# Optimization experiments

Hardware: AMD Instinct MI355X
Metric: run time of the kernel (lower is better)

## Reference

```python
import jax, jax.numpy as jnp
import numpy as np

B = 262144      # batch of Monte Carlo paths
D = 5           # number of assets
NSTEPS = 20     # Euler-Maruyama steps
H = 0.1         # T / N
R = 0.06        # risk-free rate
T = 2.0
SIGMA = 0.2     # vol (same for all assets)
B_DRIFT = 0.1   # P-measure drift
CURTAGE = 0.005
SQRT_H = float(np.sqrt(H))


def setup_inputs() -> dict:
    key = jax.random.key(0)
    ks = jax.random.split(key, 10)
    sc = 0.1  # weight init scale
    return {
        "x_in": jax.random.uniform(ks[0], (B, 1), dtype=jnp.float32),
        "dW": jax.random.normal(ks[1], (NSTEPS, B, D), dtype=jnp.float32) * SQRT_H,
        "Wo": jax.random.normal(ks[2], (1, 2 * D + 1), dtype=jnp.float32) * sc,
        "bo": jnp.zeros((2 * D + 1,), jnp.float32),
        "Wk": jax.random.normal(ks[3], (1, 2 * D), dtype=jnp.float32) * sc,
        "bk": jnp.zeros((2 * D,), jnp.float32),
        "Wu0": jax.random.normal(ks[4], (1, D), dtype=jnp.float32) * sc,
        "bu0": jnp.zeros((D,), jnp.float32),
        "W1": jax.random.normal(ks[5], (NSTEPS - 1, 1, 20), dtype=jnp.float32) * sc,
        "b1": jnp.zeros((NSTEPS - 1, 20), jnp.float32),
        "W2": jax.random.normal(ks[6], (NSTEPS - 1, 20, 20), dtype=jnp.float32) * sc,
        "b2": jnp.zeros((NSTEPS - 1, 20), jnp.float32),
        "W3": jax.random.normal(ks[7], (NSTEPS - 1, 20, D), dtype=jnp.float32) * sc,
        "b3": jnp.zeros((NSTEPS - 1, D), jnp.float32),
    }


def _mlp(x, w1, c1, w2, c2, w3, c3):
    # SubNetwork: Dense(20) relu -> Dense(20) relu -> Dense(D) linear
    h1 = jax.nn.relu(x @ w1 + c1)
    h2 = jax.nn.relu(h1 @ w2 + c2)
    return h2 @ w3 + c3


def _forward(x_in, dW, Wo, bo, Wk, bk, Wu0, bu0, W1, b1, W2, b2, W3, b3):
    b_vec = jnp.full((D,), B_DRIFT, dtype=x_in.dtype)
    x = x_in                                             # wealth [B,1]
    alpha_options = jax.nn.softmax(x @ Wo + bo, axis=-1)[:, : 2 * D]
    alpha_options_tot = jnp.mean(jnp.sum(alpha_options, axis=1))
    K = 1.0 + 0.25 * jnp.tanh(x @ Wk + bk)               # strikes [B,2D]
    rescale = 1.0 - alpha_options_tot
    alpha = x @ Wu0 + bu0                                # linear head, [B,D]

    S = jnp.ones((x.shape[0], D), dtype=x.dtype)         # P-measure asset prices
    S_Q = S                                              # Q-measure asset prices
    dN_acu = jnp.zeros((x.shape[0], D), dtype=x.dtype)
    N_m1 = None

    for n in range(1, NSTEPS + 1):   # fixed small unrolled rollout
        u = alpha                                        # dollar allocation per asset
        N_p = u / S                                      # number of shares
        if n > 1:
            dN_acu = dN_acu + jnp.abs(N_p - N_m1)        # turnover accumulator
        N_m1 = N_p
        dWn = dW[n - 1]
        # wealth Euler step: risk-free on cash + risky exposure (GBM, no jumps)
        x = x + (x - jnp.sum(u, axis=1, keepdims=True)) * (R * H) \
              + jnp.sum(u * (b_vec * H + SIGMA * dWn), axis=1, keepdims=True)
        S = S * (1.0 + b_vec * H + SIGMA * dWn)
        S_Q = S_Q * (1.0 + R * H + SIGMA * dWn)
        if n < NSTEPS:
            alpha = _mlp(x, W1[n - 1], b1[n - 1], W2[n - 1], b2[n - 1],
                         W3[n - 1], b3[n - 1])

    dN = jnp.sum(dN_acu, axis=1, keepdims=True)          # [B,1]
    disc = jnp.exp(-R * T)
    C0 = disc * jnp.mean(jnp.maximum(S_Q - K[:, :D], 0.0), axis=0)   # [D] MC call price
    P0 = disc * jnp.mean(jnp.maximum(K[:, D:] - S_Q, 0.0), axis=0)   # [D] MC put price
    C_T = jnp.maximum(S - K[:, :D], 0.0) / (C0 + 1e-8)
    P_T = jnp.maximum(K[:, D:] - S, 0.0) / (P0 + 1e-8)
    del P_T  # options_in_p=False: puts/calls not added to wealth

    x = x - CURTAGE * dN                                 # transaction costs

    p5 = jnp.percentile(x, 5.0)
    p95 = jnp.percentile(x, 95.0)
    m_lo = x < p5
    m_hi = x > p95
    cnt_lo = jnp.maximum(jnp.sum(m_lo), 1).astype(x.dtype)
    cnt_hi = jnp.maximum(jnp.sum(m_hi), 1).astype(x.dtype)

    loss1 = -jnp.mean(x)
    loss2 = jnp.var(x)
    loss3 = -jnp.sum(jnp.where(m_lo, x, 0.0)) / cnt_lo   # -CVaR_5 tail mean
    loss4 = -jnp.sum(jnp.where(m_hi, x, 0.0)) / cnt_hi
    loss5 = jnp.mean(C_T[:, 0])
    loss6 = K[0, 1]
    loss7 = jnp.asarray(rescale, x.dtype)
    return (loss1, loss2, loss3, loss4, loss5, loss6, loss7)


def reference(x_in, dW, Wo, bo, Wk, bk, Wu0, bu0, W1, b1, W2, b2, W3, b3):
    losses = _forward(x_in, dW, Wo, bo, Wk, bk, Wu0, bu0,
                      W1, b1, W2, b2, W3, b3)
    return tuple(jnp.reshape(l, (1,)) for l in losses)
```

## Files before the change

### kernel.cpp

```cpp
#include <hip/hip_runtime.h>
#include <math.h>

#define BB 262144
#define NST 20
#define RHc 0.006f
#define BHc 0.01f
#define SIGc 0.2f
#define CURTc 0.005f
#define DISCf 0.8869204367171575f

#define P 4
#define THB 256
#define NBLK_SIM 256
#define CH 65536

#define H1_BLK 32
#define H1_THR 1024
#define W_BLK 256
#define W_THR 256

#define SIMP_OFF  BB
#define TAILP_OFF (SIMP_OFF + NBLK_SIM * 5)
#define ICTRL     (TAILP_OFF + W_BLK * 4)
#define H2_OFF 0
#define H3_OFF 8192
#define CNT_OFF 12288
#define ST_OFF  12296
#define SF_OFF  12320
#define ZTOT    12289
#define H1R_OFF 12352

__device__ __forceinline__ unsigned fkey(float f) {
    unsigned u = __float_as_uint(f);
    return (u & 0x80000000u) ? ~u : (u | 0x80000000u);
}
__device__ __forceinline__ float funkey(unsigned k) {
    return __uint_as_float((k & 0x80000000u) ? (k ^ 0x80000000u) : ~k);
}
__device__ __forceinline__ float wred(float v) {
#pragma unroll
    for (int o = 32; o > 0; o >>= 1) v += __shfl_down(v, o);
    return v;
}
__device__ __forceinline__ unsigned short f2bf(float f) {
    unsigned u = __float_as_uint(f);
    unsigned r = u + 0x7fffu + ((u >> 16) & 1u);
    return (unsigned short)(r >> 16);
}

__global__ void zero_kernel(int* __restrict__ ctrl) {
    int i = blockIdx.x * blockDim.x + threadIdx.x;
    if (i < ZTOT) ctrl[i] = 0;
}

#define STRD 416
#define HB   (19 * STRD)

__global__ __launch_bounds__(THB, 1) void sim_kernel(
    const float* __restrict__ x_in, const float* __restrict__ dW,
    const float* __restrict__ Wo, const float* __restrict__ bo,
    const float* __restrict__ Wk, const float* __restrict__ bk,
    const float* __restrict__ Wu0, const float* __restrict__ bu0,
    const float* __restrict__ W1, const float* __restrict__ b1,
    const float* __restrict__ W2, const float* __restrict__ b2,
    const float* __restrict__ W3, const float* __restrict__ b3,
    float* __restrict__ ws, int* __restrict__ ctrl, float* __restrict__ out)
{
    __shared__ float L[HB + 40];
    __shared__ float red[4][5];
    __shared__ int lastF;
    const int tid = threadIdx.x;

    for (int t = tid; t < 19 * 20; t += THB) {
        int s = t / 20, j = t % 20;
        L[s * STRD + j]      = W1[t];
        L[s * STRD + 20 + j] = b1[t];
        L[s * STRD + 40 + j] = b2[t];
    }
    for (int t = tid; t < 19 * 100; t += THB) {
        int s = t / 100, r = t % 100, i = r / 5, k = r % 5;
        L[s * STRD + 60 + k * 20 + i] = W3[t];
    }
    for (int t = tid; t < 19 * 5; t += THB) {
        int s = t / 5, k = t % 5;
        L[s * STRD + 160 + k] = b3[t];
    }
    {
        unsigned short* Ls16 = (unsigned short*)L;
        for (int t = tid; t < 19 * 400; t += THB) {
            int s = t / 400, r = t % 400, i = r / 20, j = r % 20;
            Ls16[(s * STRD + 168 + i * 12) * 2 + j] = f2bf(W2[t]);
        }
        for (int t = tid; t < 19 * 80; t += THB) {
            int s = t / 80, r = t % 80, i = r / 4, q = r % 4;
            Ls16[(s * STRD + 168 + i * 12) * 2 + 20 + q] = 0;
        }
    }
    if (tid < 11) { L[HB + tid] = Wo[tid]; L[HB + 11 + tid] = bo[tid]; }
    if (tid == 0) { L[HB + 22] = Wk[0]; L[HB + 23] = bk[0]; }
    if (tid < 5)  { L[HB + 24 + tid] = Wu0[tid]; L[HB + 29 + tid] = bu0[tid]; }
    __syncthreads();

    const int b0 = blockIdx.x * THB + tid;

    float x[P], K0[P], SQ0[P], dNs[P], smv = 0.f;
    float alpha[P][5], S[P][5], Nm1[P][5], dwb[P][5];

#pragma unroll
    for (int p = 0; p < P; p++) {
        int b = b0 + p * CH;
        float xx = x_in[b];
        x[p] = xx;
        float z[11], zm = -1e30f;
#pragma unroll
        for (int j = 0; j < 11; j++) {
            z[j] = fmaf(xx, L[HB + j], L[HB + 11 + j]);
            zm = fmaxf(zm, z[j]);
        }
        float se = 0.f;
#pragma unroll
        for (int j = 0; j < 11; j++) se += __expf(z[j] - zm);
        smv += __expf(z[10] - zm) / se;
        K0[p] = 1.f + 0.25f * tanhf(fmaf(xx, L[HB + 22], L[HB + 23]));
        SQ0[p] = 1.f; dNs[p] = 0.f;
#pragma unroll
        for (int d = 0; d < 5; d++) {
            alpha[p][d] = fmaf(xx, L[HB + 24 + d], L[HB + 29 + d]);
            S[p][d] = 1.f;
            Nm1[p][d] = alpha[p][d];
        }
        const float* pw = dW + (size_t)b * 5;
#pragma unroll
        for (int d = 0; d < 5; d++) dwb[p][d] = pw[d];
    }

#pragma unroll 1
    for (int n = 1; n <= NST; n++) {
        float dwc[P][5];
#pragma unroll
        for (int p = 0; p < P; p++)
#pragma unroll
            for (int d = 0; d < 5; d++) dwc[p][d] = dwb[p][d];
        if (n < NST) {
#pragma unroll
            for (int p = 0; p < P; p++) {
                const float* pw = dW + ((size_t)n * BB + b0 + p * CH) * 5;
#pragma unroll
                for (int d = 0; d < 5; d++) dwb[p][d] = pw[d];
            }
        }
#pragma unroll
        for (int p = 0; p < P; p++) {
            float usum = 0.f, du = 0.f, dn = 0.f;
#pragma unroll
            for (int d = 0; d < 5; d++) {
                float u = alpha[p][d];
                float Np = u * __builtin_amdgcn_rcpf(S[p][d]);
                dn += fabsf(Np - Nm1[p][d]);
                Nm1[p][d] = Np;
                usum += u;
                du = fmaf(u, fmaf(SIGc, dwc[p][d], BHc), du);
            }
            dNs[p] += dn;
            x[p] = fmaf(x[p] - usum, RHc, x[p]) + du;
#pragma unroll
            for (int d = 0; d < 5; d++)
                S[p][d] *= (1.f + BHc + SIGc * dwc[p][d]);
            SQ0[p] *= (1.f + RHc + SIGc * dwc[p][0]);
        }
        if (n < NST) {
            const float* Ls = L + (n - 1) * STRD;
            float h2[P][20];
#pragma unroll
            for (int j4 = 0; j4 < 5; j4++) {
                float4 c = *(const float4*)(Ls + 40 + j4 * 4);
#pragma unroll
                for (int p = 0; p < P; p++) {
                    h2[p][j4 * 4 + 0] = c.x; h2[p][j4 * 4 + 1] = c.y;
                    h2[p][j4 * 4 + 2] = c.z; h2[p][j4 * 4 + 3] = c.w;
                }
            }
#pragma unroll 1
            for (int i4 = 0; i4 < 5; i4++) {
                float4 w1c = *(const float4*)(Ls + i4 * 4);
                float4 c1c = *(const float4*)(Ls + 20 + i4 * 4);
#pragma unroll
                for (int ii = 0; ii < 4; ii++) {
                    int i = i4 * 4 + ii;
                    const uint4 q0 = *(const uint4*)(Ls + 168 + i * 12);
                    const uint4 q1 = *(const uint4*)(Ls + 168 + i * 12 + 4);
                    const uint2 q2 = *(const uint2*)(Ls + 168 + i * 12 + 8);
                    float w[20];
                    w[0]  = __uint_as_float(q0.x << 16); w[1]  = __uint_as_float(q0.x & 0xffff0000u);
                    w[2]  = __uint_as_float(q0.y << 16); w[3]  = __uint_as_float(q0.y & 0xffff0000u);
                    w[4]  = __uint_as_float(q0.z << 16); w[5]  = __uint_as_float(q0.z & 0xffff0000u);
                    w[6]  = __uint_as_float(q0.w << 16); w[7]  = __uint_as_float(q0.w & 0xffff0000u);
                    w[8]  = __uint_as_float(q1.x << 16); w[9]  = __uint_as_float(q1.x & 0xffff0000u);
                    w[10] = __uint_as_float(q1.y << 16); w[11] = __uint_as_float(q1.y & 0xffff0000u);
                    w[12] = __uint_as_float(q1.z << 16); w[13] = __uint_as_float(q1.z & 0xffff0000u);
                    w[14] = __uint_as_float(q1.w << 16); w[15] = __uint_as_float(q1.w & 0xffff0000u);
                    w[16] = __uint_as_float(q2.x << 16); w[17] = __uint_as_float(q2.x & 0xffff0000u);
                    w[18] = __uint_as_float(q2.y << 16); w[19] = __uint_as_float(q2.y & 0xffff0000u);
                    float wv = (ii == 0) ? w1c.x : (ii == 1) ? w1c.y : (ii == 2) ? w1c.z : w1c.w;
                    float cv = (ii == 0) ? c1c.x : (ii == 1) ? c1c.y : (ii == 2) ? c1c.z : c1c.w;
#pragma unroll
                    for (int p = 0; p < P; p++) {
                        float hv = fmaxf(fmaf(x[p], wv, cv), 0.f);
#pragma unroll
                        for (int j = 0; j < 20; j++)
                            h2[p][j] = fmaf(hv, w[j], h2[p][j]);
                    }
                }
            }
#pragma unroll
            for (int p = 0; p < P; p++)
#pragma unroll
                for (int j = 0; j < 20; j++) h2[p][j] = fmaxf(h2[p][j], 0.f);
#pragma unroll
            for (int k = 0; k < 5; k++) {
                const float* wr = Ls + 60 + k * 20;
                float4 wa  = *(const float4*)(wr + 0);
                float4 wb2 = *(const float4*)(wr + 4);
                float4 wc2 = *(const float4*)(wr + 8);
                float4 wd2 = *(const float4*)(wr + 12);
                float4 we2 = *(const float4*)(wr + 16);
                float bb = Ls[160 + k];
#pragma unroll
                for (int p = 0; p < P; p++) {
                    float a = bb;
                    a = fmaf(h2[p][0], wa.x, a);  a = fmaf(h2[p][1], wa.y, a);
                    a = fmaf(h2[p][2], wa.z, a);  a = fmaf(h2[p][3], wa.w, a);
                    a = fmaf(h2[p][4], wb2.x, a); a = fmaf(h2[p][5], wb2.y, a);
                    a = fmaf(h2[p][6], wb2.z, a); a = fmaf(h2[p][7], wb2.w, a);
                    a = fmaf(h2[p][8], wc2.x, a); a = fmaf(h2[p][9], wc2.y, a);
                    a = fmaf(h2[p][10], wc2.z, a); a = fmaf(h2[p][11], wc2.w, a);
                    a = fmaf(h2[p][12], wd2.x, a); a = fmaf(h2[p][13], wd2.y, a);
                    a = fmaf(h2[p][14], wd2.z, a); a = fmaf(h2[p][15], wd2.w, a);
                    a = fmaf(h2[p][16], we2.x, a); a = fmaf(h2[p][17], we2.y, a);
                    a = fmaf(h2[p][18], we2.z, a); a = fmaf(h2[p][19], we2.w, a);
                    alpha[p][k] = a;
                }
            }
        }
    }

    float v0 = 0.f, v1 = 0.f, v2 = 0.f, v3 = 0.f, v4 = smv;
#pragma unroll
    for (int p = 0; p < P; p++) {
        float xx = fmaf(-CURTc, dNs[p], x[p]);
        ws[b0 + p * CH] = xx;
        v0 += xx; v1 += xx * xx;
        v2 += fmaxf(S[p][0] - K0[p], 0.f);
        v3 += fmaxf(SQ0[p]  - K0[p], 0.f);
    }

    v0 = wred(v0); v1 = wred(v1); v2 = wred(v2); v3 = wred(v3); v4 = wred(v4);
    int wid = tid >> 6, lane = tid & 63;
    if (lane == 0) { red[wid][0] = v0; red[wid][1] = v1; red[wid][2] = v2; red[wid][3] = v3; red[wid][4] = v4; }
    __syncthreads();
    if (tid == 0) {
        float s0 = 0, s1 = 0, s2 = 0, s3 = 0, s4 = 0;
#pragma unroll
        for (int w = 0; w < 4; w++) { s0 += red[w][0]; s1 += red[w][1]; s2 += red[w][2]; s3 += red[w][3]; s4 += red[w][4]; }
        float* part = ws + SIMP_OFF + blockIdx.x * 5;
        part[0] = s0; part[1] = s1; part[2] = s2; part[3] = s3; part[4] = s4;
    }
    __threadfence();
    if (tid == 0) lastF = (atomicAdd(&ctrl[CNT_OFF], 1) == NBLK_SIM - 1);
    __syncthreads();
    if (!lastF) return;
    __threadfence();

    const float* part = ws + SIMP_OFF;
    float a0 = part[tid * 5 + 0], a1 = part[tid * 5 + 1], a2 = part[tid * 5 + 2],
          a3 = part[tid * 5 + 3], a4 = part[tid * 5 + 4];
    a0 = wred(a0); a1 = wred(a1); a2 = wred(a2); a3 = wred(a3); a4 = wred(a4);
    if (lane == 0) { red[wid][0] = a0; red[wid][1] = a1; red[wid][2] = a2; red[wid][3] = a3; red[wid][4] = a4; }
    __syncthreads();
    if (tid == 0) {
        float Sx = 0, Sx2 = 0, SP = 0, SQs = 0, Ssm = 0;
#pragma unroll
        for (int w = 0; w < 4; w++) { Sx += red[w][0]; Sx2 += red[w][1]; SP += red[w][2]; SQs += red[w][3]; Ssm += red[w][4]; }
        float invB = 1.f / (float)BB;
        float meanx = Sx * invB;
        out[0] = -meanx;
        out[1] = Sx2 * invB - meanx * meanx;
        out[4] = (SP * invB) / (DISCf * (SQs * invB) + 1e-8f);
        out[5] = 1.f + 0.25f * tanhf(fmaf(x_in[0], Wk[1], bk[1]));
        out[6] = Ssm * invB;
    }
}

__device__ __forceinline__ void aggAdd(int* h, int code) {
    bool act = (code >= 0);
    unsigned long long mask = __ballot(act);
    while (mask) {
        int leader = __ffsll((unsigned long long)mask) - 1;
        int lc = __shfl(code, leader);
        unsigned long long mm = __ballot(act && code == lc);
        if ((threadIdx.x & 63) == leader) atomicAdd(&h[lc], (int)__popcll(mm));
        mask &= ~mm;
    }
}

__device__ int excl_scan1024(int v, int tid, int* wsum) {
    __syncthreads();
    int lane = tid & 63, wid = tid >> 6;
    int inc = v;
#pragma unroll
    for (int o = 1; o < 64; o <<= 1) { int u = __shfl_up(inc, o); if (lane >= o) inc += u; }
    if (lane == 63) wsum[wid] = inc;
    __syncthreads();
    if (tid < 16) {
        int wv = wsum[tid], winc = wv;
#pragma unroll
        for (int o = 1; o < 16; o <<= 1) { int u = __shfl_up(winc, o); if (tid >= o) winc += u; }
        wsum[tid] = winc - wv;
    }
    __syncthreads();
    return wsum[wid] + inc - v;
}

__global__ __launch_bounds__(H1_THR) void hist1_kernel(const float* __restrict__ xf,
                                                       int* __restrict__ ctrl)
{
    __shared__ int lh[2048];
    const int tid = threadIdx.x, bl = blockIdx.x;
    for (int i = tid; i < 2048; i += H1_THR) lh[i] = 0;
    __syncthreads();
    const float4* xf4 = (const float4*)xf;
#pragma unroll
    for (int w = 0; w < 2; w++) {
        float4 v = xf4[(size_t)bl * 2048 + w * 1024 + tid];
        aggAdd(lh, (int)(fkey(v.x) >> 21));
        aggAdd(lh, (int)(fkey(v.y) >> 21));
        aggAdd(lh, (int)(fkey(v.z) >> 21));
        aggAdd(lh, (int)(fkey(v.w) >> 21));
    }
    __syncthreads();
    int* row = ctrl + H1R_OFF + bl * 2048;
    for (int i = tid; i < 2048; i += H1_THR) row[i] = lh[i];
}

__global__ __launch_bounds__(1024) void scan1_kernel(int* __restrict__ ctrl)
{
    __shared__ int wsum[16];
    __shared__ int binT[4], remT[4];
    const int tid = threadIdx.x;
    const int* rows = ctrl + H1R_OFF;
    int c0 = 0, c1 = 0;
    for (int r = 0; r < H1_BLK; r++) {
        c0 += rows[r * 2048 + 2 * tid];
        c1 += rows[r * 2048 + 2 * tid + 1];
    }
    int s = c0 + c1;
    int E = excl_scan1024(s, tid, wsum);
    const int RK[4] = {13107, 13108, 249035, 249036};
#pragma unroll
    for (int t = 0; t < 4; t++) {
        int r = RK[t];
        if (r >= E && r < E + s) {
            if (r < E + c0) { binT[t] = 2 * tid;     remT[t] = r - E; }
            else            { binT[t] = 2 * tid + 1; remT[t] = r - E - c0; }
        }
    }
    __syncthreads();
    if (tid == 0) {
        for (int t = 0; t < 4; t++) { ctrl[ST_OFF + t] = binT[t]; ctrl[ST_OFF + 4 + t] = remT[t]; }
        for (int t = 0; t < 4; t++) {
            int g = t;
            for (int q = 0; q < t; q++) if (binT[q] == binT[t]) { g = q; break; }
            ctrl[ST_OFF + 8 + t] = g;
        }
    }
}

__global__ __launch_bounds__(W_THR) void hist2_kernel(const float* __restrict__ xf,
                                                      int* __restrict__ ctrl)
{
    const int tid = threadIdx.x, bl = blockIdx.x;
    int pf[4], gp[4];
#pragma unroll
    for (int t = 0; t < 4; t++) { pf[t] = ctrl[ST_OFF + t]; gp[t] = ctrl[ST_OFF + 8 + t]; }
    float4 v = ((const float4*)xf)[(size_t)bl * W_THR + tid];
    float xv[4] = {v.x, v.y, v.z, v.w};
#pragma unroll
    for (int k = 0; k < 4; k++) {
        unsigned u = fkey(xv[k]);
        unsigned hi = u >> 21;
        int bin = (int)((u >> 10) & 2047u);
        int code = -1;
#pragma unroll
        for (int t = 0; t < 4; t++)
            if (gp[t] == t && (unsigned)pf[t] == hi) code = t * 2048 + bin;
        aggAdd(ctrl + H2_OFF, code);
    }
}

__global__ __launch_bounds__(1024) void scan2_kernel(int* __restrict__ ctrl)
{
    __shared__ int wsum[16];
    __shared__ int binT[4], remT[4];
    const int tid = threadIdx.x;
    for (int t = 0; t < 4; t++) {
        int g = ctrl[ST_OFF + 8 + t], rank = ctrl[ST_OFF + 4 + t];
        const int* h = ctrl + H2_OFF + g * 2048;
        int c0 = h[2 * tid], c1 = h[2 * tid + 1];
        int s = c0 + c1;
        int E = excl_scan1024(s, tid, wsum);
        if (rank >= E && rank < E + s) {
            if (rank < E + c0) { binT[t] = 2 * tid;     remT[t] = rank - E; }
            else               { binT[t] = 2 * tid + 1; remT[t] = rank - E - c0; }
        }
        __syncthreads();
    }
    if (tid == 0) {
        int P2n[4];
        for (int t = 0; t < 4; t++) {
            P2n[t] = (ctrl[ST_OFF + t] << 11) | binT[t];
            ctrl[ST_OFF + 12 + t] = P2n[t];
            ctrl[ST_OFF + 16 + t] = remT[t];
        }
        for (int t = 0; t < 4; t++) {
            int g = t;
            for (int q = 0; q < t; q++) if (P2n[q] == P2n[t]) { g = q; break; }
            ctrl[ST_OFF + 20 + t] = g;
        }
    }
}

__global__ __launch_bounds__(W_THR) void hist3_kernel(const float* __restrict__ xf,
                                                      int* __restrict__ ctrl)
{
    const int tid = threadIdx.x, bl = blockIdx.x;
    int pf[4], gp[4];
#pragma unroll
    for (int t = 0; t < 4; t++) { pf[t] = ctrl[ST_OFF + 12 + t]; gp[t] = ctrl[ST_OFF + 20 + t]; }
    float4 v = ((const float4*)xf)[(size_t)bl * W_THR + tid];
    float xv[4] = {v.x, v.y, v.z, v.w};
#pragma unroll
    for (int k = 0; k < 4; k++) {
        unsigned u = fkey(xv[k]);
        unsigned hi = u >> 10;
        int bin = (int)(u & 1023u);
        int code = -1;
#pragma unroll
        for (int t = 0; t < 4; t++)
            if (gp[t] == t && (unsigned)pf[t] == hi) code = t * 1024 + bin;
        aggAdd(ctrl + H3_OFF, code);
    }
}

__global__ __launch_bounds__(1024) void scan3_kernel(int* __restrict__ ctrl)
{
    __shared__ int wsum[16];
    __shared__ int binT[4];
    const int tid = threadIdx.x;
    for (int t = 0; t < 4; t++) {
        int g = ctrl[ST_OFF + 20 + t], rank = ctrl[ST_OFF + 16 + t];
        const int* h = ctrl + H3_OFF + g * 1024;
        int s = h[tid];
        int E = excl_scan1024(s, tid, wsum);
        if (rank >= E && rank < E + s) binT[t] = tid;
        __syncthreads();
    }
    if (tid == 0) {
        float* sf = (float*)(ctrl + SF_OFF);
        float v[4];
        for (int t = 0; t < 4; t++) {
            unsigned key = ((unsigned)ctrl[ST_OFF + 12 + t] << 10) | (unsigned)binT[t];
            v[t] = funkey(key);
            sf[t] = v[t];
        }
        sf[4] = v[0] + 0.15f * (v[1] - v[0]);
        sf[5] = v[2] + 0.85f * (v[3] - v[2]);
    }
}

__global__ __launch_bounds__(W_THR) void tail_kernel(const float* __restrict__ xf,
                                                     const int* __restrict__ ctrl,
                                                     float* __restrict__ ws)
{
    __shared__ float frd[4][4];
    const int tid = threadIdx.x, bl = blockIdx.x;
    const float* sf = (const float*)(ctrl + SF_OFF);
    const float p5 = sf[4], p95 = sf[5];
    float4 v = ((const float4*)xf)[(size_t)bl * W_THR + tid];
    float xv[4] = {v.x, v.y, v.z, v.w};
    float slo = 0.f, clo = 0.f, shi = 0.f, chi = 0.f;
#pragma unroll
    for (int k = 0; k < 4; k++) {
        float x = xv[k];
        if (x < p5)  { slo += x; clo += 1.f; }
        if (x > p95) { shi += x; chi += 1.f; }
    }
    slo = wred(slo); clo = wred(clo); shi = wred(shi); chi = wred(chi);
    int wid = tid >> 6, lane = tid & 63;
    if (lane == 0) { frd[wid][0] = slo; frd[wid][1] = clo; frd[wid][2] = shi; frd[wid][3] = chi; }
    __syncthreads();
    if (tid == 0) {
        float s0 = 0, s1 = 0, s2 = 0, s3 = 0;
#pragma unroll
        for (int w = 0; w < 4; w++) { s0 += frd[w][0]; s1 += frd[w][1]; s2 += frd[w][2]; s3 += frd[w][3]; }
        float* tp = ws + TAILP_OFF + bl * 4;
        tp[0] = s0; tp[1] = s1; tp[2] = s2; tp[3] = s3;
    }
}

__global__ __launch_bounds__(256) void tailfin_kernel(const float* __restrict__ ws,
                                                      float* __restrict__ out)
{
    __shared__ float frd[4][4];
    const int tid = threadIdx.x;
    const float* tp = ws + TAILP_OFF;
    float a0 = tp[tid * 4 + 0], a1 = tp[tid * 4 + 1], a2 = tp[tid * 4 + 2], a3 = tp[tid * 4 + 3];
    a0 = wred(a0); a1 = wred(a1); a2 = wred(a2); a3 = wred(a3);
    int wid = tid >> 6, lane = tid & 63;
    if (lane == 0) { frd[wid][0] = a0; frd[wid][1] = a1; frd[wid][2] = a2; frd[wid][3] = a3; }
    __syncthreads();
    if (tid == 0) {
        float Slo = 0, Clo = 0, Shi = 0, Chi = 0;
#pragma unroll
        for (int w = 0; w < 4; w++) { Slo += frd[w][0]; Clo += frd[w][1]; Shi += frd[w][2]; Chi += frd[w][3]; }
        out[2] = -Slo / fmaxf(Clo, 1.f);
        out[3] = -Shi / fmaxf(Chi, 1.f);
    }
}

extern "C" void kernel_launch(void* const* d_in, const int* in_sizes, int n_in,
                              void* d_out, int out_size, void* d_ws, size_t ws_size,
                              hipStream_t stream)
{
    const float* x_in = (const float*)d_in[0];
    const float* dW   = (const float*)d_in[1];
    const float* Wo   = (const float*)d_in[2];
    const float* bo   = (const float*)d_in[3];
    const float* Wk   = (const float*)d_in[4];
    const float* bk   = (const float*)d_in[5];
    const float* Wu0  = (const float*)d_in[6];
    const float* bu0  = (const float*)d_in[7];
    const float* W1   = (const float*)d_in[8];
    const float* b1   = (const float*)d_in[9];
    const float* W2   = (const float*)d_in[10];
    const float* b2   = (const float*)d_in[11];
    const float* W3   = (const float*)d_in[12];
    const float* b3   = (const float*)d_in[13];
    float* ws  = (float*)d_ws;
    int* ctrl  = (int*)d_ws + ICTRL;
    float* out = (float*)d_out;

    zero_kernel<<<(ZTOT + 1023) / 1024, 1024, 0, stream>>>(ctrl);
    sim_kernel<<<NBLK_SIM, THB, 0, stream>>>(x_in, dW, Wo, bo, Wk, bk, Wu0, bu0,
                                             W1, b1, W2, b2, W3, b3, ws, ctrl, out);
    hist1_kernel<<<H1_BLK, H1_THR, 0, stream>>>(ws, ctrl);
    scan1_kernel<<<1, 1024, 0, stream>>>(ctrl);
    hist2_kernel<<<W_BLK, W_THR, 0, stream>>>(ws, ctrl);
    scan2_kernel<<<1, 1024, 0, stream>>>(ctrl);
    hist3_kernel<<<W_BLK, W_THR, 0, stream>>>(ws, ctrl);
    scan3_kernel<<<1, 1024, 0, stream>>>(ctrl);
    tail_kernel<<<W_BLK, W_THR, 0, stream>>>(ws, ctrl, ws);
    tailfin_kernel<<<1, 256, 0, stream>>>(ws, out);
}
```

Baseline: 192.1 us.

## Revert W2 to fp32 in shared memory, track per-asset Q prices, halve hist blocks

Layer-2 weights go back from packed bf16 to plain fp32 in shared memory with a new 568-float per-step stride. This drops the per-element unpack shifts but doubles the LDS bytes read per step. The simulation now keeps per-asset Q-measure prices and per-asset dN accumulators, which adds register pressure and extra multiplies even though only the first Q price is used. The histogram pass now runs 16 blocks that each process twice as much data, and the Wk/bk load indexing changes.

```diff
diff --git a/kernel.cpp b/kernel.cpp
--- a/kernel.cpp
+++ b/kernel.cpp
@@ -13,8 +13,7 @@
 #define THB 256
 #define NBLK_SIM 256
 #define CH 65536
-
-#define H1_BLK 32
+#define H1_BLK 16
 #define H1_THR 1024
 #define W_BLK 256
 #define W_THR 256
@@ -42,19 +41,32 @@
     for (int o = 32; o > 0; o >>= 1) v += __shfl_down(v, o);
     return v;
 }
-__device__ __forceinline__ unsigned short f2bf(float f) {
-    unsigned u = __float_as_uint(f);
-    unsigned r = u + 0x7fffu + ((u >> 16) & 1u);
-    return (unsigned short)(r >> 16);
-}
 
 __global__ void zero_kernel(int* __restrict__ ctrl) {
     int i = blockIdx.x * blockDim.x + threadIdx.x;
     if (i < ZTOT) ctrl[i] = 0;
 }
 
-#define STRD 416
-#define HB   (19 * STRD)
+#define ACC20(P_) do { \
+  h2[P_][0]=fmaf(hv,wa.x,h2[P_][0]);  h2[P_][1]=fmaf(hv,wa.y,h2[P_][1]); \
+  h2[P_][2]=fmaf(hv,wa.z,h2[P_][2]);  h2[P_][3]=fmaf(hv,wa.w,h2[P_][3]); \
+  h2[P_][4]=fmaf(hv,wb2.x,h2[P_][4]); h2[P_][5]=fmaf(hv,wb2.y,h2[P_][5]); \
+  h2[P_][6]=fmaf(hv,wb2.z,h2[P_][6]); h2[P_][7]=fmaf(hv,wb2.w,h2[P_][7]); \
+  h2[P_][8]=fmaf(hv,wc2.x,h2[P_][8]); h2[P_][9]=fmaf(hv,wc2.y,h2[P_][9]); \
+  h2[P_][10]=fmaf(hv,wc2.z,h2[P_][10]); h2[P_][11]=fmaf(hv,wc2.w,h2[P_][11]); \
+  h2[P_][12]=fmaf(hv,wd2.x,h2[P_][12]); h2[P_][13]=fmaf(hv,wd2.y,h2[P_][13]); \
+  h2[P_][14]=fmaf(hv,wd2.z,h2[P_][14]); h2[P_][15]=fmaf(hv,wd2.w,h2[P_][15]); \
+  h2[P_][16]=fmaf(hv,we2.x,h2[P_][16]); h2[P_][17]=fmaf(hv,we2.y,h2[P_][17]); \
+  h2[P_][18]=fmaf(hv,we2.z,h2[P_][18]); h2[P_][19]=fmaf(hv,we2.w,h2[P_][19]); \
+} while (0)
+
+#define DOT20(P_) do { \
+  a=fmaf(h2[P_][0],wa.x,a);  a=fmaf(h2[P_][1],wa.y,a);  a=fmaf(h2[P_][2],wa.z,a);  a=fmaf(h2[P_][3],wa.w,a); \
+  a=fmaf(h2[P_][4],wb2.x,a); a=fmaf(h2[P_][5],wb2.y,a); a=fmaf(h2[P_][6],wb2.z,a); a=fmaf(h2[P_][7],wb2.w,a); \
+  a=fmaf(h2[P_][8],wc2.x,a); a=fmaf(h2[P_][9],wc2.y,a); a=fmaf(h2[P_][10],wc2.z,a); a=fmaf(h2[P_][11],wc2.w,a); \
+  a=fmaf(h2[P_][12],wd2.x,a); a=fmaf(h2[P_][13],wd2.y,a); a=fmaf(h2[P_][14],wd2.z,a); a=fmaf(h2[P_][15],wd2.w,a); \
+  a=fmaf(h2[P_][16],we2.x,a); a=fmaf(h2[P_][17],we2.y,a); a=fmaf(h2[P_][18],we2.z,a); a=fmaf(h2[P_][19],we2.w,a); \
+} while (0)
 
 __global__ __launch_bounds__(THB, 1) void sim_kernel(
     const float* __restrict__ x_in, const float* __restrict__ dW,
@@ -66,45 +78,38 @@
     const float* __restrict__ W3, const float* __restrict__ b3,
     float* __restrict__ ws, int* __restrict__ ctrl, float* __restrict__ out)
 {
-    __shared__ float L[HB + 40];
+    __shared__ float L[10844];
     __shared__ float red[4][5];
     __shared__ int lastF;
     const int tid = threadIdx.x;
 
     for (int t = tid; t < 19 * 20; t += THB) {
         int s = t / 20, j = t % 20;
-        L[s * STRD + j]      = W1[t];
-        L[s * STRD + 20 + j] = b1[t];
-        L[s * STRD + 40 + j] = b2[t];
+        L[s * 568 + j]       = W1[t];
+        L[s * 568 + 20 + j]  = b1[t];
+        L[s * 568 + 440 + j] = b2[t];
+    }
+    for (int t = tid; t < 19 * 400; t += THB) {
+        int s = t / 400, r = t % 400;
+        L[s * 568 + 40 + r] = W2[t];
     }
     for (int t = tid; t < 19 * 100; t += THB) {
         int s = t / 100, r = t % 100, i = r / 5, k = r % 5;
-        L[s * STRD + 60 + k * 20 + i] = W3[t];
+        L[s * 568 + 460 + k * 20 + i] = W3[t];
     }
     for (int t = tid; t < 19 * 5; t += THB) {
         int s = t / 5, k = t % 5;
-        L[s * STRD + 160 + k] = b3[t];
-    }
-    {
-        unsigned short* Ls16 = (unsigned short*)L;
-        for (int t = tid; t < 19 * 400; t += THB) {
-            int s = t / 400, r = t % 400, i = r / 20, j = r % 20;
-            Ls16[(s * STRD + 168 + i * 12) * 2 + j] = f2bf(W2[t]);
-        }
-        for (int t = tid; t < 19 * 80; t += THB) {
-            int s = t / 80, r = t % 80, i = r / 4, q = r % 4;
-            Ls16[(s * STRD + 168 + i * 12) * 2 + 20 + q] = 0;
-        }
-    }
-    if (tid < 11) { L[HB + tid] = Wo[tid]; L[HB + 11 + tid] = bo[tid]; }
-    if (tid == 0) { L[HB + 22] = Wk[0]; L[HB + 23] = bk[0]; }
-    if (tid < 5)  { L[HB + 24 + tid] = Wu0[tid]; L[HB + 29 + tid] = bu0[tid]; }
+        L[s * 568 + 560 + k] = b3[t];
+    }
+    if (tid < 11) { L[10792 + tid] = Wo[tid]; L[10803 + tid] = bo[tid]; }
+    if (tid < 10) { L[10814 + tid] = Wk[tid]; L[10824 + tid] = bk[tid]; }
+    if (tid < 5)  { L[10834 + tid] = Wu0[tid]; L[10839 + tid] = bu0[tid]; }
     __syncthreads();
 
     const int b0 = blockIdx.x * THB + tid;
 
-    float x[P], K0[P], SQ0[P], dNs[P], smv = 0.f;
-    float alpha[P][5], S[P][5], Nm1[P][5], dwb[P][5];
+    float x[P], K0[P], smv = 0.f;
+    float alpha[P][5], S[P][5], SQ[P][5], dN[P][5], Nm1[P][5], dwb[P][5];
 
 #pragma unroll
     for (int p = 0; p < P; p++) {
@@ -114,19 +119,18 @@
         float z[11], zm = -1e30f;
 #pragma unroll
         for (int j = 0; j < 11; j++) {
-            z[j] = fmaf(xx, L[HB + j], L[HB + 11 + j]);
+            z[j] = fmaf(xx, L[10792 + j], L[10803 + j]);
             zm = fmaxf(zm, z[j]);
         }
         float se = 0.f;
 #pragma unroll
         for (int j = 0; j < 11; j++) se += __expf(z[j] - zm);
         smv += __expf(z[10] - zm) / se;
-        K0[p] = 1.f + 0.25f * tanhf(fmaf(xx, L[HB + 22], L[HB + 23]));
-        SQ0[p] = 1.f; dNs[p] = 0.f;
+        K0[p] = 1.f + 0.25f * tanhf(fmaf(xx, L[10814], L[10824]));
 #pragma unroll
         for (int d = 0; d < 5; d++) {
-            alpha[p][d] = fmaf(xx, L[HB + 24 + d], L[HB + 29 + d]);
-            S[p][d] = 1.f;
+            alpha[p][d] = fmaf(xx, L[10834 + d], L[10839 + d]);
+            S[p][d] = 1.f; SQ[p][d] = 1.f; dN[p][d] = 0.f;
             Nm1[p][d] = alpha[p][d];
         }
         const float* pw = dW + (size_t)b * 5;
@@ -151,29 +155,30 @@
         }
 #pragma unroll
         for (int p = 0; p < P; p++) {
-            float usum = 0.f, du = 0.f, dn = 0.f;
+            float usum = 0.f, du = 0.f;
 #pragma unroll
             for (int d = 0; d < 5; d++) {
                 float u = alpha[p][d];
                 float Np = u * __builtin_amdgcn_rcpf(S[p][d]);
-                dn += fabsf(Np - Nm1[p][d]);
+                dN[p][d] += fabsf(Np - Nm1[p][d]);
                 Nm1[p][d] = Np;
                 usum += u;
                 du = fmaf(u, fmaf(SIGc, dwc[p][d], BHc), du);
             }
-            dNs[p] += dn;
             x[p] = fmaf(x[p] - usum, RHc, x[p]) + du;
 #pragma unroll
-            for (int d = 0; d < 5; d++)
-                S[p][d] *= (1.f + BHc + SIGc * dwc[p][d]);
-            SQ0[p] *= (1.f + RHc + SIGc * dwc[p][0]);
+            for (int d = 0; d < 5; d++) {
+                float g = SIGc * dwc[p][d];
+                S[p][d]  *= (1.f + BHc + g);
+                SQ[p][d] *= (1.f + RHc + g);
+            }
         }
         if (n < NST) {
-            const float* Ls = L + (n - 1) * STRD;
+            const float* Ls = L + (n - 1) * 568;
             float h2[P][20];
 #pragma unroll
             for (int j4 = 0; j4 < 5; j4++) {
-                float4 c = *(const float4*)(Ls + 40 + j4 * 4);
+                float4 c = *(const float4*)(Ls + 440 + j4 * 4);
 #pragma unroll
                 for (int p = 0; p < P; p++) {
                     h2[p][j4 * 4 + 0] = c.x; h2[p][j4 * 4 + 1] = c.y;
@@ -184,31 +189,21 @@
             for (int i4 = 0; i4 < 5; i4++) {
                 float4 w1c = *(const float4*)(Ls + i4 * 4);
                 float4 c1c = *(const float4*)(Ls + 20 + i4 * 4);
+                const float* wr0 = Ls + 40 + i4 * 80;
 #pragma unroll
                 for (int ii = 0; ii < 4; ii++) {
-                    int i = i4 * 4 + ii;
-                    const uint4 q0 = *(const uint4*)(Ls + 168 + i * 12);
-                    const uint4 q1 = *(const uint4*)(Ls + 168 + i * 12 + 4);
-                    const uint2 q2 = *(const uint2*)(Ls + 168 + i * 12 + 8);
-                    float w[20];
-                    w[0]  = __uint_as_float(q0.x << 16); w[1]  = __uint_as_float(q0.x & 0xffff0000u);
-                    w[2]  = __uint_as_float(q0.y << 16); w[3]  = __uint_as_float(q0.y & 0xffff0000u);
-                    w[4]  = __uint_as_float(q0.z << 16); w[5]  = __uint_as_float(q0.z & 0xffff0000u);
-                    w[6]  = __uint_as_float(q0.w << 16); w[7]  = __uint_as_float(q0.w & 0xffff0000u);
-                    w[8]  = __uint_as_float(q1.x << 16); w[9]  = __uint_as_float(q1.x & 0xffff0000u);
-                    w[10] = __uint_as_float(q1.y << 16); w[11] = __uint_as_float(q1.y & 0xffff0000u);
-                    w[12] = __uint_as_float(q1.z << 16); w[13] = __uint_as_float(q1.z & 0xffff0000u);
-                    w[14] = __uint_as_float(q1.w << 16); w[15] = __uint_as_float(q1.w & 0xffff0000u);
-                    w[16] = __uint_as_float(q2.x << 16); w[17] = __uint_as_float(q2.x & 0xffff0000u);
-                    w[18] = __uint_as_float(q2.y << 16); w[19] = __uint_as_float(q2.y & 0xffff0000u);
+                    const float* wr = wr0 + ii * 20;
+                    float4 wa  = *(const float4*)(wr + 0);
+                    float4 wb2 = *(const float4*)(wr + 4);
+                    float4 wc2 = *(const float4*)(wr + 8);
+                    float4 wd2 = *(const float4*)(wr + 12);
+                    float4 we2 = *(const float4*)(wr + 16);
                     float wv = (ii == 0) ? w1c.x : (ii == 1) ? w1c.y : (ii == 2) ? w1c.z : w1c.w;
                     float cv = (ii == 0) ? c1c.x : (ii == 1) ? c1c.y : (ii == 2) ? c1c.z : c1c.w;
 #pragma unroll
                     for (int p = 0; p < P; p++) {
                         float hv = fmaxf(fmaf(x[p], wv, cv), 0.f);
-#pragma unroll
-                        for (int j = 0; j < 20; j++)
-                            h2[p][j] = fmaf(hv, w[j], h2[p][j]);
+                        ACC20(p);
                     }
                 }
             }
@@ -218,26 +213,17 @@
                 for (int j = 0; j < 20; j++) h2[p][j] = fmaxf(h2[p][j], 0.f);
 #pragma unroll
             for (int k = 0; k < 5; k++) {
-                const float* wr = Ls + 60 + k * 20;
+                const float* wr = Ls + 460 + k * 20;
                 float4 wa  = *(const float4*)(wr + 0);
                 float4 wb2 = *(const float4*)(wr + 4);
                 float4 wc2 = *(const float4*)(wr + 8);
                 float4 wd2 = *(const float4*)(wr + 12);
                 float4 we2 = *(const float4*)(wr + 16);
-                float bb = Ls[160 + k];
+                float bb = Ls[560 + k];
 #pragma unroll
                 for (int p = 0; p < P; p++) {
                     float a = bb;
-                    a = fmaf(h2[p][0], wa.x, a);  a = fmaf(h2[p][1], wa.y, a);
-                    a = fmaf(h2[p][2], wa.z, a);  a = fmaf(h2[p][3], wa.w, a);
-                    a = fmaf(h2[p][4], wb2.x, a); a = fmaf(h2[p][5], wb2.y, a);
-                    a = fmaf(h2[p][6], wb2.z, a); a = fmaf(h2[p][7], wb2.w, a);
-                    a = fmaf(h2[p][8], wc2.x, a); a = fmaf(h2[p][9], wc2.y, a);
-                    a = fmaf(h2[p][10], wc2.z, a); a = fmaf(h2[p][11], wc2.w, a);
-                    a = fmaf(h2[p][12], wd2.x, a); a = fmaf(h2[p][13], wd2.y, a);
-                    a = fmaf(h2[p][14], wd2.z, a); a = fmaf(h2[p][15], wd2.w, a);
-                    a = fmaf(h2[p][16], we2.x, a); a = fmaf(h2[p][17], we2.y, a);
-                    a = fmaf(h2[p][18], we2.z, a); a = fmaf(h2[p][19], we2.w, a);
+                    DOT20(p);
                     alpha[p][k] = a;
                 }
             }
@@ -247,11 +233,12 @@
     float v0 = 0.f, v1 = 0.f, v2 = 0.f, v3 = 0.f, v4 = smv;
 #pragma unroll
     for (int p = 0; p < P; p++) {
-        float xx = fmaf(-CURTc, dNs[p], x[p]);
+        float dNs = dN[p][0] + dN[p][1] + dN[p][2] + dN[p][3] + dN[p][4];
+        float xx = fmaf(-CURTc, dNs, x[p]);
         ws[b0 + p * CH] = xx;
         v0 += xx; v1 += xx * xx;
-        v2 += fmaxf(S[p][0] - K0[p], 0.f);
-        v3 += fmaxf(SQ0[p]  - K0[p], 0.f);
+        v2 += fmaxf(S[p][0]  - K0[p], 0.f);
+        v3 += fmaxf(SQ[p][0] - K0[p], 0.f);
     }
 
     v0 = wred(v0); v1 = wred(v1); v2 = wred(v2); v3 = wred(v3); v4 = wred(v4);
@@ -330,8 +317,8 @@
     __syncthreads();
     const float4* xf4 = (const float4*)xf;
 #pragma unroll
-    for (int w = 0; w < 2; w++) {
-        float4 v = xf4[(size_t)bl * 2048 + w * 1024 + tid];
+    for (int w = 0; w < 4; w++) {
+        float4 v = xf4[(size_t)bl * 4096 + w * 1024 + tid];
         aggAdd(lh, (int)(fkey(v.x) >> 21));
         aggAdd(lh, (int)(fkey(v.y) >> 21));
         aggAdd(lh, (int)(fkey(v.z) >> 21));
```

Measured after the change: 198.2 us. +3.2%, slower.
